# Kernel optimization log

Measured on AMD Instinct MI355X. Metric: run time of the kernel, lower is better.

## Reference

```python
import jax, jax.numpy as jnp
import numpy as np

B, T, C_EMB, HEAD = 8, 2048, 1024, 64

def setup_inputs() -> dict:
    key = jax.random.key(0)
    kx, kq, kk, kv = jax.random.split(key, 4)
    x = jax.random.normal(kx, (B, T, C_EMB), dtype=jnp.float32)
    s = 1.0 / np.sqrt(C_EMB)
    Wq = jax.random.normal(kq, (C_EMB, HEAD), dtype=jnp.float32) * s
    Wk = jax.random.normal(kk, (C_EMB, HEAD), dtype=jnp.float32) * s
    Wv = jax.random.normal(kv, (C_EMB, HEAD), dtype=jnp.float32) * s
    return {"x": x, "Wq": Wq, "Wk": Wk, "Wv": Wv}


def _apply_rotary(q, k):
    # q, k: [B, T, D] with D = head_size; matches torch apply_rotary_emb
    D = q.shape[-1]
    pos = jnp.arange(q.shape[1], dtype=jnp.float32)                # [T]
    dim_arr = jnp.arange(0, D, 2, dtype=jnp.float32)               # [D/2]
    freqs = 10000.0 ** (-dim_arr / D)                              # [D/2]
    theta = pos[:, None] * freqs[None, :]                          # [T, D/2]
    cos = jnp.concatenate([jnp.cos(theta), jnp.cos(theta)], -1)[None]  # [1,T,D]
    sin = jnp.concatenate([jnp.sin(theta), jnp.sin(theta)], -1)[None]

    def rot(v):
        v1, v2 = v[..., : D // 2], v[..., D // 2 :]
        return jnp.concatenate([-v2, v1], axis=-1)

    return q * cos + rot(q) * sin, k * cos + rot(k) * sin


def reference(x, Wq, Wk, Wv):
    Bx, Tx, Cx = x.shape
    q = x @ Wq  # [B,T,H]
    k = x @ Wk
    v = x @ Wv
    q, k = _apply_rotary(q, k)
    # NOTE: original scales by C**-0.5 where C = n_embd, not head_size
    scale = Cx ** (-0.5)
    wei = jnp.einsum("bqd,bkd->bqk", q, k) * scale                 # [B,T,T]
    causal = jnp.tril(jnp.ones((Tx, Tx), dtype=bool))
    wei = jnp.where(causal[None], wei, -jnp.inf)
    wei = jax.nn.softmax(wei, axis=-1)
    out = jnp.einsum("bqk,bkd->bqd", wei, v)                       # [B,T,H]
    return out
```

## Files before the change

### kernel.cpp

```cpp
#include <hip/hip_runtime.h>

typedef __bf16 bf16x8 __attribute__((ext_vector_type(8)));
typedef float f32x4 __attribute__((ext_vector_type(4)));
typedef unsigned short u16;

#define MFMA __builtin_amdgcn_mfma_f32_16x16x32_bf16

__device__ __forceinline__ u16 f2bf_bits(float f) {
  unsigned u = __builtin_bit_cast(unsigned, f);
  u = (u + 0x7fffu + ((u >> 16) & 1u)) >> 16;
  return (u16)u;
}
__device__ __forceinline__ __bf16 f2bf(float f) {
  u16 b = f2bf_bits(f);
  return __builtin_bit_cast(__bf16, b);
}
__device__ __forceinline__ float bf2f(u16 b) {
  return __builtin_bit_cast(float, (unsigned)b << 16);
}

__device__ __forceinline__ int swz_off(int row, int col) {
  return row * 64 + ((((col >> 3) ^ row) & 7) << 3) + (col & 7);
}
__device__ __forceinline__ bf16x8 lds_read8(const __bf16* buf, int row, int col) {
  return *(const bf16x8*)(buf + (row * 64 + ((((col >> 3) ^ row) & 7) << 3)));
}
__device__ __forceinline__ void lds_write8(__bf16* buf, int row, int col, bf16x8 v) {
  *(bf16x8*)(buf + (row * 64 + ((((col >> 3) ^ row) & 7) << 3))) = v;
}

__global__ __launch_bounds__(256) void prep_w_kernel(
    const float* __restrict__ Wq, const float* __restrict__ Wk,
    const float* __restrict__ Wv, u16* __restrict__ wtg) {
  int idx = blockIdx.x * 256 + threadIdx.x;
  if (idx >= 192 * 1024) return;
  int row = idx >> 10, k = idx & 1023;
  const float* W = (row < 64) ? Wq : ((row < 128) ? Wk : Wv);
  int col = row & 63;
  wtg[idx] = f2bf_bits(W[(size_t)k * 64 + col]);
}

__device__ __forceinline__ void rope2(f32x4& lo, f32x4& hi, int i, float t_base) {
  float f = __expf(-(float)i * 0.28782313662425572f);
#pragma unroll
  for (int r = 0; r < 4; ++r) {
    float th = (t_base + (float)r) * f;
    float sn, cs;
    sincosf(th, &sn, &cs);
    float L = lo[r], H = hi[r];
    lo[r] = L * cs - H * sn;
    hi[r] = H * cs + L * sn;
  }
}

__global__ __launch_bounds__(512) void qkv_rope_kernel(
    const float* __restrict__ x, const u16* __restrict__ wtg,
    u16* __restrict__ qg, u16* __restrict__ kg, u16* __restrict__ vtg) {
  __shared__ __bf16 xbuf[2][64 * 64];
  __shared__ __bf16 wbuf[2][192 * 64];
  const int tid = threadIdx.x;
  const int w = tid >> 6, l = tid & 63;
  const int wr = w >> 1, wc = w & 1;
  const int lr = l & 15, lg = l >> 4;
  const int r0 = blockIdx.x * 64;
  const int b = r0 >> 11, t0 = r0 & 2047;

  f32x4 acc[6];
#pragma unroll
  for (int j = 0; j < 6; ++j) acc[j] = (f32x4){0.f, 0.f, 0.f, 0.f};

  const int srow = tid >> 3, sc8 = tid & 7;
  const float* xbase = x + (size_t)(r0 + srow) * 1024 + sc8 * 8;

  float4 xA0, xA1, xB0, xB1;
  bf16x8 swr[3];

  auto loadW = [&](int k0) {
#pragma unroll
    for (int s = 0; s < 3; ++s) {
      int id = tid + s * 512;
      swr[s] = *(const bf16x8*)(wtg + (size_t)(id >> 3) * 1024 + k0 + (id & 7) * 8);
    }
  };
  auto writeW = [&](int bsel) {
#pragma unroll
    for (int s = 0; s < 3; ++s) {
      int id = tid + s * 512;
      lds_write8(wbuf[bsel], id >> 3, (id & 7) * 8, swr[s]);
    }
  };
  auto writeX = [&](int bsel, float4 a0, float4 a1) {
    bf16x8 v;
    v[0] = f2bf(a0.x); v[1] = f2bf(a0.y); v[2] = f2bf(a0.z); v[3] = f2bf(a0.w);
    v[4] = f2bf(a1.x); v[5] = f2bf(a1.y); v[6] = f2bf(a1.z); v[7] = f2bf(a1.w);
    lds_write8(xbuf[bsel], srow, sc8 * 8, v);
  };

  xA0 = *(const float4*)xbase;
  xA1 = *(const float4*)(xbase + 4);
  loadW(0);
  writeX(0, xA0, xA1);
  writeW(0);
  xB0 = *(const float4*)(xbase + 64);
  xB1 = *(const float4*)(xbase + 68);
  __syncthreads();

#pragma unroll
  for (int s = 0; s < 16; ++s) {
    const int cur = s & 1;
    if (s < 14) {
      const float* p = xbase + (size_t)(s + 2) * 64;
      if (cur == 0) { xA0 = *(const float4*)p; xA1 = *(const float4*)(p + 4); }
      else          { xB0 = *(const float4*)p; xB1 = *(const float4*)(p + 4); }
    }
    if (s < 15) loadW((s + 1) * 64);
#pragma unroll
    for (int kk = 0; kk < 2; ++kk) {
      bf16x8 a = lds_read8(xbuf[cur], wr * 16 + lr, kk * 32 + lg * 8);
#pragma unroll
      for (int j = 0; j < 6; ++j) {
        constexpr int TM[2][6] = {{0, 1, 2, 3, 4, 6}, {5, 7, 8, 9, 10, 11}};
        int tl = TM[wc][j];
        bf16x8 bb = lds_read8(wbuf[cur], tl * 16 + lr, kk * 32 + lg * 8);
        acc[j] = MFMA(a, bb, acc[j], 0, 0, 0);
      }
    }
    if (s < 15) {
      if (cur == 0) writeX(1, xB0, xB1);
      else          writeX(0, xA0, xA1);
      writeW(cur ^ 1);
      __syncthreads();
    }
  }

  const float t_base = (float)(t0 + wr * 16 + lg * 4);
  if (wc == 0) {
    rope2(acc[0], acc[2], lr, t_base);
    rope2(acc[1], acc[3], 16 + lr, t_base);
    rope2(acc[4], acc[5], lr, t_base);
#pragma unroll
    for (int j = 0; j < 4; ++j)
#pragma unroll
      for (int r = 0; r < 4; ++r) {
        float qv = acc[j][r] * 0.03125f;
        qg[(size_t)(r0 + wr * 16 + lg * 4 + r) * 64 + j * 16 + lr] = f2bf_bits(qv);
      }
#pragma unroll
    for (int r = 0; r < 4; ++r) {
      size_t rowo = (size_t)(r0 + wr * 16 + lg * 4 + r) * 64;
      kg[rowo + lr] = f2bf_bits(acc[4][r]);
      kg[rowo + 32 + lr] = f2bf_bits(acc[5][r]);
    }
  } else {
    rope2(acc[0], acc[1], 16 + lr, t_base);
#pragma unroll
    for (int r = 0; r < 4; ++r) {
      size_t rowo = (size_t)(r0 + wr * 16 + lg * 4 + r) * 64;
      kg[rowo + 16 + lr] = f2bf_bits(acc[0][r]);
      kg[rowo + 48 + lr] = f2bf_bits(acc[1][r]);
    }
#pragma unroll
    for (int j = 2; j < 6; ++j) {
      int d = (j - 2) * 16 + lr;
      ushort4 uv;
      uv.x = f2bf_bits(acc[j][0]);
      uv.y = f2bf_bits(acc[j][1]);
      uv.z = f2bf_bits(acc[j][2]);
      uv.w = f2bf_bits(acc[j][3]);
      *(ushort4*)(vtg + (size_t)(b * 64 + d) * 2048 + t0 + wr * 16 + lg * 4) = uv;
    }
  }
}

__global__ __launch_bounds__(256) void attn_part_kernel(
    const u16* __restrict__ qg, const u16* __restrict__ kg,
    const u16* __restrict__ vtg, u16* __restrict__ opart,
    float* __restrict__ lpart, float* __restrict__ out, int CT, int NCH) {
  const int idx = blockIdx.x;
  const int b = idx / (32 * NCH);
  const int rem = idx % (32 * NCH);
  const int qt = rem / NCH, ch = rem % NCH;
  const int t0v = ch * CT;
  if (t0v > qt) return;
  const int t1v = min(qt + 1, t0v + CT);
  const int nv = qt / CT + 1;

  __shared__ __bf16 kbuf[2][64 * 64];
  __shared__ __bf16 vbuf[2][64 * 64];
  __shared__ __bf16 pbuf[4 * 16 * 64];
  const int tid = threadIdx.x;
  const int w = tid >> 6, l = tid & 63;
  const int lr = l & 15, lg = l >> 4;
  const int q0 = qt * 64;
  const float NEG_INF = -__builtin_inff();

  const u16* qrow = qg + (size_t)(b * 2048 + q0 + w * 16 + lr) * 64;
  bf16x8 qf0 = *(const bf16x8*)(qrow + lg * 8);
  bf16x8 qf1 = *(const bf16x8*)(qrow + 32 + lg * 8);

  bf16x8 kr[2], vr[2];
  auto stage_load = [&](int c) {
#pragma unroll
    for (int s = 0; s < 2; ++s) {
      int id = tid + s * 256;
      int row = id >> 3, c8 = id & 7;
      kr[s] = *(const bf16x8*)(kg + (size_t)(b * 2048 + c * 64 + row) * 64 + c8 * 8);
      vr[s] = *(const bf16x8*)(vtg + (size_t)(b * 64 + row) * 2048 + c * 64 + c8 * 8);
    }
  };
  auto stage_write = [&](int bsel) {
#pragma unroll
    for (int s = 0; s < 2; ++s) {
      int id = tid + s * 256;
      int row = id >> 3, c8 = id & 7;
      lds_write8(kbuf[bsel], row, c8 * 8, kr[s]);
      lds_write8(vbuf[bsel], row, c8 * 8, vr[s]);
    }
  };

  f32x4 acc_o[4];
#pragma unroll
  for (int n = 0; n < 4; ++n) acc_o[n] = (f32x4){0.f, 0.f, 0.f, 0.f};
  float l_p[4] = {0.f, 0.f, 0.f, 0.f};

  stage_load(t0v);
  stage_write(0);
  __syncthreads();

  for (int c = t0v; c < t1v; ++c) {
    const int cur = (c - t0v) & 1;
    const bool more = (c + 1 < t1v);
    if (more) stage_load(c + 1);

    f32x4 s4[4];
#pragma unroll
    for (int nt = 0; nt < 4; ++nt) {
      bf16x8 k0 = lds_read8(kbuf[cur], nt * 16 + lr, lg * 8);
      bf16x8 k1 = lds_read8(kbuf[cur], nt * 16 + lr, 32 + lg * 8);
      f32x4 t = (f32x4){0.f, 0.f, 0.f, 0.f};
      t = MFMA(qf0, k0, t, 0, 0, 0);
      t = MFMA(qf1, k1, t, 0, 0, 0);
      s4[nt] = t;
    }
    if (c == qt) {
#pragma unroll
      for (int nt = 0; nt < 4; ++nt)
#pragma unroll
        for (int r = 0; r < 4; ++r) {
          int kv = nt * 16 + lr, qq = w * 16 + lg * 4 + r;
          if (kv > qq) s4[nt][r] = NEG_INF;
        }
    }
    __bf16* pw = pbuf + w * (16 * 64);
#pragma unroll
    for (int nt = 0; nt < 4; ++nt)
#pragma unroll
      for (int r = 0; r < 4; ++r) {
        float p = __expf(s4[nt][r] - 8.0f);
        l_p[r] += p;
        pw[swz_off(lg * 4 + r, nt * 16 + lr)] = f2bf(p);
      }
#pragma unroll
    for (int h = 0; h < 2; ++h) {
      bf16x8 pf = lds_read8(pw, lr, h * 32 + lg * 8);
#pragma unroll
      for (int nt = 0; nt < 4; ++nt) {
        bf16x8 vf = lds_read8(vbuf[cur], nt * 16 + lr, h * 32 + lg * 8);
        acc_o[nt] = MFMA(pf, vf, acc_o[nt], 0, 0, 0);
      }
    }
    if (more) {
      stage_write(cur ^ 1);
      __syncthreads();
    }
  }

  float lsum[4];
#pragma unroll
  for (int r = 0; r < 4; ++r) {
    float s = l_p[r];
    s += __shfl_xor(s, 1);
    s += __shfl_xor(s, 2);
    s += __shfl_xor(s, 4);
    s += __shfl_xor(s, 8);
    lsum[r] = s;
  }

  if (nv == 1) {
#pragma unroll
    for (int r = 0; r < 4; ++r) {
      float inv = 1.0f / lsum[r];
      size_t rowo = (size_t)(b * 2048 + q0 + w * 16 + lg * 4 + r) * 64;
#pragma unroll
      for (int nt = 0; nt < 4; ++nt)
        out[rowo + nt * 16 + lr] = acc_o[nt][r] * inv;
    }
    return;
  }

  const size_t slot = (size_t)(b * 32 + qt) * NCH + ch;
  u16* oslot = opart + slot * 4096;
#pragma unroll
  for (int r = 0; r < 4; ++r) {
    int row = w * 16 + lg * 4 + r;
#pragma unroll
    for (int nt = 0; nt < 4; ++nt)
      oslot[row * 64 + nt * 16 + lr] = f2bf_bits(acc_o[nt][r]);
    if (lr == 0) lpart[slot * 64 + row] = lsum[r];
  }
}

__global__ __launch_bounds__(256) void attn_combine_kernel(
    const u16* __restrict__ opart, const float* __restrict__ lpart,
    float* __restrict__ out, int CT, int NCH) {
  const int bq = blockIdx.x >> 2;
  const int quarter = blockIdx.x & 3;
  const int b = bq >> 5, qt = bq & 31;
  const int nv = qt / CT + 1;
  if (nv == 1) return;
  const int row = quarter * 16 + (threadIdx.x >> 4);
  const int col = (threadIdx.x & 15) * 4;
  const size_t slot0 = (size_t)(b * 32 + qt) * NCH;

  float denom = 0.f;
  float acc[4] = {0.f, 0.f, 0.f, 0.f};
  for (int c = 0; c < nv; ++c) {
    denom += lpart[(slot0 + c) * 64 + row];
    ushort4 pv = *(const ushort4*)(opart + (slot0 + c) * 4096 + row * 64 + col);
    acc[0] += bf2f(pv.x);
    acc[1] += bf2f(pv.y);
    acc[2] += bf2f(pv.z);
    acc[3] += bf2f(pv.w);
  }
  float inv = 1.0f / denom;
  float4 o;
  o.x = acc[0] * inv; o.y = acc[1] * inv; o.z = acc[2] * inv; o.w = acc[3] * inv;
  *(float4*)(out + ((size_t)(b * 2048 + qt * 64 + row)) * 64 + col) = o;
}

extern "C" void kernel_launch(void* const* d_in, const int* in_sizes, int n_in,
                              void* d_out, int out_size, void* d_ws, size_t ws_size,
                              hipStream_t stream) {
  const float* x = (const float*)d_in[0];
  const float* Wq = (const float*)d_in[1];
  const float* Wk = (const float*)d_in[2];
  const float* Wv = (const float*)d_in[3];
  float* out = (float*)d_out;
  char* ws = (char*)d_ws;
  u16* wtg = (u16*)ws;
  u16* qg = (u16*)(ws + 393216);
  u16* kg = (u16*)(ws + 393216 + 2097152);
  u16* vtg = (u16*)(ws + 393216 + 2u * 2097152);
  const size_t base = 393216 + 3u * 2097152;
  int NCH = 8;
  while (NCH > 1 && base + (size_t)256 * NCH * 8448 > ws_size) NCH >>= 1;
  const int CT = 32 / NCH;
  u16* opart = (u16*)(ws + base);
  float* lpart = (float*)(ws + base + (size_t)256 * NCH * 8192);

  prep_w_kernel<<<dim3(768), dim3(256), 0, stream>>>(Wq, Wk, Wv, wtg);
  qkv_rope_kernel<<<dim3(256), dim3(512), 0, stream>>>(x, wtg, qg, kg, vtg);
  attn_part_kernel<<<dim3(8 * 32 * NCH), dim3(256), 0, stream>>>(
      qg, kg, vtg, opart, lpart, out, CT, NCH);
  attn_combine_kernel<<<dim3(256 * 4), dim3(256), 0, stream>>>(opart, lpart, out, CT, NCH);
}
```

Measured before the change: 54.24 us.

## Retile QKV projection warps to 32x48 and use hardware sin/cos for RoPE

The QKV+RoPE kernel now splits its 8 waves as 2 row groups by 4 column groups instead of 4 by 2. Each wave computes two 16-row tiles against three weight tiles, so every B fragment read from LDS is reused across two MFMAs. This cuts LDS reads per MFMA and balances the RoPE/epilogue work evenly across waves. RoPE also replaces sincosf with a range reduction in revolutions plus the hardware sin/cos builtins, which drops the slow-path argument reduction but may lose accuracy for large angles.

Result: no change. 53.22 us (-1.9%).

```diff
diff --git a/kernel.cpp b/kernel.cpp
--- a/kernel.cpp
+++ b/kernel.cpp
@@ -42,11 +42,13 @@
 
 __device__ __forceinline__ void rope2(f32x4& lo, f32x4& hi, int i, float t_base) {
   float f = __expf(-(float)i * 0.28782313662425572f);
+  const float inv2pi = 0.15915494309189535f;
 #pragma unroll
   for (int r = 0; r < 4; ++r) {
-    float th = (t_base + (float)r) * f;
-    float sn, cs;
-    sincosf(th, &sn, &cs);
+    float rev = (t_base + (float)r) * f * inv2pi;
+    rev = __builtin_amdgcn_fractf(rev);
+    float sn = __builtin_amdgcn_sinf(rev);
+    float cs = __builtin_amdgcn_cosf(rev);
     float L = lo[r], H = hi[r];
     lo[r] = L * cs - H * sn;
     hi[r] = H * cs + L * sn;
@@ -60,14 +62,18 @@
   __shared__ __bf16 wbuf[2][192 * 64];
   const int tid = threadIdx.x;
   const int w = tid >> 6, l = tid & 63;
-  const int wr = w >> 1, wc = w & 1;
+  const int wrg = w & 1;
+  const int wcg = w >> 1;
   const int lr = l & 15, lg = l >> 4;
   const int r0 = blockIdx.x * 64;
   const int b = r0 >> 11, t0 = r0 & 2047;
-
-  f32x4 acc[6];
-#pragma unroll
-  for (int j = 0; j < 6; ++j) acc[j] = (f32x4){0.f, 0.f, 0.f, 0.f};
+  constexpr int TM4[4][3] = {{0, 2, 8}, {1, 3, 9}, {4, 6, 10}, {5, 7, 11}};
+
+  f32x4 acc[2][3];
+#pragma unroll
+  for (int rg = 0; rg < 2; ++rg)
+#pragma unroll
+    for (int j = 0; j < 3; ++j) acc[rg][j] = (f32x4){0.f, 0.f, 0.f, 0.f};
 
   const int srow = tid >> 3, sc8 = tid & 7;
   const float* xbase = x + (size_t)(r0 + srow) * 1024 + sc8 * 8;
@@ -116,13 +122,13 @@
     if (s < 15) loadW((s + 1) * 64);
 #pragma unroll
     for (int kk = 0; kk < 2; ++kk) {
-      bf16x8 a = lds_read8(xbuf[cur], wr * 16 + lr, kk * 32 + lg * 8);
-#pragma unroll
-      for (int j = 0; j < 6; ++j) {
-        constexpr int TM[2][6] = {{0, 1, 2, 3, 4, 6}, {5, 7, 8, 9, 10, 11}};
-        int tl = TM[wc][j];
-        bf16x8 bb = lds_read8(wbuf[cur], tl * 16 + lr, kk * 32 + lg * 8);
-        acc[j] = MFMA(a, bb, acc[j], 0, 0, 0);
+      bf16x8 a0 = lds_read8(xbuf[cur], wrg * 32 + lr, kk * 32 + lg * 8);
+      bf16x8 a1 = lds_read8(xbuf[cur], wrg * 32 + 16 + lr, kk * 32 + lg * 8);
+#pragma unroll
+      for (int j = 0; j < 3; ++j) {
+        bf16x8 bb = lds_read8(wbuf[cur], TM4[wcg][j] * 16 + lr, kk * 32 + lg * 8);
+        acc[0][j] = MFMA(a0, bb, acc[0][j], 0, 0, 0);
+        acc[1][j] = MFMA(a1, bb, acc[1][j], 0, 0, 0);
       }
     }
     if (s < 15) {
@@ -133,41 +139,35 @@
     }
   }
 
-  const float t_base = (float)(t0 + wr * 16 + lg * 4);
-  if (wc == 0) {
-    rope2(acc[0], acc[2], lr, t_base);
-    rope2(acc[1], acc[3], 16 + lr, t_base);
-    rope2(acc[4], acc[5], lr, t_base);
-#pragma unroll
-    for (int j = 0; j < 4; ++j)
+  const int ph = (wcg & 1) * 16 + lr;
+#pragma unroll
+  for (int rg = 0; rg < 2; ++rg) {
+    const int rowb = wrg * 32 + rg * 16 + lg * 4;
+    const float t_base = (float)(t0 + rowb);
+    rope2(acc[rg][0], acc[rg][1], ph, t_base);
+    if (wcg < 2) {
 #pragma unroll
       for (int r = 0; r < 4; ++r) {
-        float qv = acc[j][r] * 0.03125f;
-        qg[(size_t)(r0 + wr * 16 + lg * 4 + r) * 64 + j * 16 + lr] = f2bf_bits(qv);
-      }
-#pragma unroll
-    for (int r = 0; r < 4; ++r) {
-      size_t rowo = (size_t)(r0 + wr * 16 + lg * 4 + r) * 64;
-      kg[rowo + lr] = f2bf_bits(acc[4][r]);
-      kg[rowo + 32 + lr] = f2bf_bits(acc[5][r]);
-    }
-  } else {
-    rope2(acc[0], acc[1], 16 + lr, t_base);
-#pragma unroll
-    for (int r = 0; r < 4; ++r) {
-      size_t rowo = (size_t)(r0 + wr * 16 + lg * 4 + r) * 64;
-      kg[rowo + 16 + lr] = f2bf_bits(acc[0][r]);
-      kg[rowo + 48 + lr] = f2bf_bits(acc[1][r]);
-    }
-#pragma unroll
-    for (int j = 2; j < 6; ++j) {
-      int d = (j - 2) * 16 + lr;
+        size_t rowo = (size_t)(r0 + rowb + r) * 64;
+        qg[rowo + ph] = f2bf_bits(acc[rg][0][r] * 0.03125f);
+        qg[rowo + 32 + ph] = f2bf_bits(acc[rg][1][r] * 0.03125f);
+      }
+    } else {
+#pragma unroll
+      for (int r = 0; r < 4; ++r) {
+        size_t rowo = (size_t)(r0 + rowb + r) * 64;
+        kg[rowo + ph] = f2bf_bits(acc[rg][0][r]);
+        kg[rowo + 32 + ph] = f2bf_bits(acc[rg][1][r]);
+      }
+    }
+    {
+      const int d = (TM4[wcg][2] - 8) * 16 + lr;
       ushort4 uv;
-      uv.x = f2bf_bits(acc[j][0]);
-      uv.y = f2bf_bits(acc[j][1]);
-      uv.z = f2bf_bits(acc[j][2]);
-      uv.w = f2bf_bits(acc[j][3]);
-      *(ushort4*)(vtg + (size_t)(b * 64 + d) * 2048 + t0 + wr * 16 + lg * 4) = uv;
+      uv.x = f2bf_bits(acc[rg][2][0]);
+      uv.y = f2bf_bits(acc[rg][2][1]);
+      uv.z = f2bf_bits(acc[rg][2][2]);
+      uv.w = f2bf_bits(acc[rg][2][3]);
+      *(ushort4*)(vtg + (size_t)(b * 64 + d) * 2048 + t0 + rowb) = uv;
     }
   }
 }
```
